# Performance work log

Measured on AMD Instinct MI355X. Metric: run time of the kernel, lower is better.

## Reference

```python
import jax, jax.numpy as jnp
import numpy as np

N = 50000      # nodes
E = 800000     # edges (avg degree 16)
IN = 128       # in_feats
OUT = 128      # out_feats
ASSIGN = 256   # assign_dim = B graphs * 8 clusters
B = 32         # batch_size (num graphs)


def setup_inputs() -> dict:
    key = jax.random.key(0)
    k0, k1, k2, k3 = jax.random.split(key, 4)
    x = jax.random.normal(k0, (N, IN), jnp.float32)
    edge_index = jax.random.randint(k1, (2, E), 0, N, dtype=jnp.int32)
    # sorted graph ids, ~equal-sized graphs (mirrors block_diag mask construction)
    batch = ((jnp.arange(N, dtype=jnp.int32) * B) // N).astype(jnp.int32)
    # SAGEConv params: Linear(2*in_feats -> out) on concat([x, mean_neigh])
    W_embed = jax.random.normal(k2, (2 * IN, OUT), jnp.float32) / np.float32(np.sqrt(2 * IN))
    b_embed = jnp.zeros((OUT,), jnp.float32)
    W_pool = jax.random.normal(k3, (2 * IN, ASSIGN), jnp.float32) / np.float32(np.sqrt(2 * IN))
    b_pool = jnp.zeros((ASSIGN,), jnp.float32)
    return dict(x=x, edge_index=edge_index, batch=batch,
                W_embed=W_embed, b_embed=b_embed, W_pool=W_pool, b_pool=b_pool)


def _sage(x, src, dst, W, b):
    # mean aggregation over in-neighbors (messages src -> dst), then Linear on concat
    n = x.shape[0]
    deg = jax.ops.segment_sum(jnp.ones((src.shape[0],), x.dtype), dst, num_segments=n)
    neigh = jax.ops.segment_sum(x[src], dst, num_segments=n) / jnp.maximum(deg, 1.0)[:, None]
    return jnp.concatenate([x, neigh], axis=-1) @ W + b


def reference(x, edge_index, batch, W_embed, b_embed, W_pool, b_pool):
    src, dst = edge_index[0], edge_index[1]
    embed = _sage(x, src, dst, W_embed, b_embed)                      # [N, OUT]
    pooled = jax.nn.softmax(_sage(x, src, dst, W_pool, b_pool), -1)   # [N, ASSIGN]
    # block-diagonal mask: node i of graph g sees columns [g*C, (g+1)*C)
    C = ASSIGN // B
    cols = jnp.arange(ASSIGN, dtype=batch.dtype) // C
    mask = (batch[:, None] == cols[None, :]).astype(x.dtype)          # [N, ASSIGN]
    # NOTE: faithful to original: softmax of (mask * pooled), zeros contribute exp(0)
    r = jax.nn.softmax(mask * pooled, axis=-1) * mask
    r = r / (r.sum(axis=-1, keepdims=True) + 1e-13)                   # [N, ASSIGN]
    h = r.T @ embed                                                   # [ASSIGN, OUT]
    # adj_new = S^T A S with A sparse COO (rows=edge_index[0], cols=edge_index[1])
    ar = jax.ops.segment_sum(r[dst], src, num_segments=x.shape[0])    # A @ S : [N, ASSIGN]
    adj_new = r.T @ ar                                                # [ASSIGN, ASSIGN]
    return (adj_new, h)
```

## Files before the change

### kernel.cpp

```cpp
#include <hip/hip_runtime.h>
#include <hip/hip_bf16.h>

#define N_ 50000
#define E_ 800000
#define IN_ 128
#define OUT_ 128
#define ASSIGN_ 256
#define B_ 32
#define KTOT 256
#define JTOT 384
#define HCHUNK 32
#define ACHUNK 32
#define AST 72
#define NXP ((N_ + 127) / 128)
#define NGB (NXP * 3)

#define NBKT 128
#define NPB 391
#define BCAP 7000
#define EPB 4096
#define NBLK_A ((E_ + EPB - 1) / EPB)

typedef __attribute__((ext_vector_type(8))) short short8;
typedef __attribute__((ext_vector_type(4))) float f32x4;
typedef __attribute__((ext_vector_type(2))) float f32x2;
typedef __attribute__((ext_vector_type(4))) unsigned short ushort4v;
typedef __attribute__((ext_vector_type(2))) unsigned short ushort2v;
typedef unsigned short u16;

__device__ inline unsigned short f2bf(float v) {
    union { float f; unsigned u; } a;
    a.f = v;
    unsigned r = a.u + 0x7fff + ((a.u >> 16) & 1);
    return (unsigned short)(r >> 16);
}
__device__ inline float bf2f(unsigned short b) {
    union { unsigned u; float f; } a;
    a.u = ((unsigned)b) << 16;
    return a.f;
}

__device__ inline unsigned enc8(float v) {
    union { float f; unsigned u; } a;
    a.f = v * 0x1p-120f;
    unsigned b = a.u;
    unsigned r = b + 0x7FFFF + ((b >> 20) & 1);
    return ((r >> 20) & 0x7F) | ((b >> 24) & 0x80);
}
__device__ inline float2 dec8x2(unsigned short p) {
#if defined(__has_builtin) && __has_builtin(__builtin_amdgcn_cvt_pk_f32_fp8)
    f32x2 r = __builtin_amdgcn_cvt_pk_f32_fp8((int)(unsigned)p, false);
    return make_float2(r.x, r.y);
#else
    unsigned u0 = p & 0xffu, u1 = (p >> 8) & 0xffu;
    union { unsigned u; float f; } a, b;
    a.u = ((u0 & 0x80u) << 24) | ((u0 & 0x7fu) << 20);
    b.u = ((u1 & 0x80u) << 24) | ((u1 & 0x7fu) << 20);
    return make_float2(a.f * 0x1p+120f, b.f * 0x1p+120f);
#endif
}

__global__ __launch_bounds__(256) void k_convx(const float* __restrict__ x,
                                               unsigned short* __restrict__ xhi,
                                               unsigned char* __restrict__ xq,
                                               int* __restrict__ bktFill) {
    if (blockIdx.x == 0 && threadIdx.x < NBKT) bktFill[threadIdx.x] = threadIdx.x * BCAP;
    int i4 = (blockIdx.x * 256 + threadIdx.x) * 4;
    if (i4 >= N_ * 128) return;
    float4 v = *(const float4*)(x + i4);
    ushort4v h;
    h.x = f2bf(v.x); h.y = f2bf(v.y); h.z = f2bf(v.z); h.w = f2bf(v.w);
    *(ushort4v*)(xhi + i4) = h;
    unsigned q = enc8(v.x) | (enc8(v.y) << 8) | (enc8(v.z) << 16) | (enc8(v.w) << 24);
    *(unsigned*)(xq + i4) = q;
}

__global__ __launch_bounds__(256) void k_binA(const int* __restrict__ ei,
                                              int* __restrict__ bktFill,
                                              int2* __restrict__ ebkt) {
    __shared__ int lh[NBKT], lbase[NBKT], lofs[NBKT];
    int t = threadIdx.x;
    int e0 = blockIdx.x * EPB;
    if (t < NBKT) { lh[t] = 0; lofs[t] = 0; }
    __syncthreads();
    int ss[16], dd[16];
#pragma unroll
    for (int i = 0; i < 16; i++) {
        int e = e0 + i * 256 + t;
        ss[i] = 0; dd[i] = -1;
        if (e < E_) {
            ss[i] = ei[e];
            dd[i] = ei[E_ + e];
            atomicAdd(&lh[dd[i] / NPB], 1);
        }
    }
    __syncthreads();
    if (t < NBKT) lbase[t] = atomicAdd(&bktFill[t], lh[t]);
    __syncthreads();
#pragma unroll
    for (int i = 0; i < 16; i++) {
        if (dd[i] >= 0) {
            int b = dd[i] / NPB;
            int o = atomicAdd(&lofs[b], 1);
            ebkt[lbase[b] + o] = make_int2(ss[i], dd[i]);
        }
    }
}

__global__ __launch_bounds__(256) void k_binB0(const int* __restrict__ bktFill,
                                               const int2* __restrict__ ebkt,
                                               int* __restrict__ locOff,
                                               int* __restrict__ bucketTotal) {
    __shared__ int ldeg[NPB];
    __shared__ int lscan[512];
    int b = blockIdx.x, t = threadIdx.x;
    for (int i = t; i < NPB; i += 256) ldeg[i] = 0;
    __syncthreads();
    int base = b * BCAP;
    int cnt = bktFill[b] - base;
    int n0 = b * NPB;
    for (int j = t; j < cnt; j += 256)
        atomicAdd(&ldeg[ebkt[base + j].y - n0], 1);
    __syncthreads();
    lscan[t] = (t < NPB) ? ldeg[t] : 0;
    lscan[t + 256] = (t + 256 < NPB) ? ldeg[t + 256] : 0;
    __syncthreads();
    for (int off = 1; off < 512; off <<= 1) {
        int x0 = lscan[t];
        int x1 = lscan[t + 256];
        int a0 = (t >= off) ? lscan[t - off] : 0;
        int a1 = (t + 256 >= off) ? lscan[t + 256 - off] : 0;
        __syncthreads();
        lscan[t] = x0 + a0;
        lscan[t + 256] = x1 + a1;
        __syncthreads();
    }
    for (int i = t; i < NPB; i += 256) {
        int n = n0 + i;
        if (n < N_) locOff[n] = (i == 0) ? 0 : lscan[i - 1];
    }
    if (t == 0) bucketTotal[b] = lscan[NPB - 1];
}

__global__ __launch_bounds__(128) void k_scanS(const int* __restrict__ bucketTotal,
                                               int* __restrict__ bucketBase,
                                               int* __restrict__ rowStart) {
    __shared__ int sh[128];
    int t = threadIdx.x;
    sh[t] = bucketTotal[t];
    __syncthreads();
    for (int off = 1; off < 128; off <<= 1) {
        int x = sh[t];
        int a = (t >= off) ? sh[t - off] : 0;
        __syncthreads();
        sh[t] = x + a;
        __syncthreads();
    }
    bucketBase[t] = (t == 0) ? 0 : sh[t - 1];
    if (t == 0) rowStart[N_] = E_;
}

__global__ __launch_bounds__(256) void k_binB1(const int* __restrict__ bktFill,
                                               const int2* __restrict__ ebkt,
                                               const int* __restrict__ locOff,
                                               const int* __restrict__ bucketBase,
                                               int* __restrict__ rowStart,
                                               int* __restrict__ csr_src,
                                               int* __restrict__ csr_dst) {
    __shared__ int lfill[NPB];
    int b = blockIdx.x, t = threadIdx.x;
    int base0 = bucketBase[b];
    int n0 = b * NPB;
    for (int i = t; i < NPB; i += 256) {
        int n = n0 + i;
        if (n < N_) {
            int lo = locOff[n];
            lfill[i] = lo;
            rowStart[n] = base0 + lo;
        }
    }
    __syncthreads();
    int base = b * BCAP;
    int cnt = bktFill[b] - base;
    for (int j = t; j < cnt; j += 256) {
        int2 sd = ebkt[base + j];
        int p = base0 + atomicAdd(&lfill[sd.y - n0], 1);
        csr_src[p] = sd.x;
        csr_dst[p] = sd.y;
    }
}

__global__ __launch_bounds__(256) void k_agg(const unsigned char* __restrict__ xq,
                                             const int* __restrict__ rowStart,
                                             const int* __restrict__ csr_src,
                                             unsigned short* __restrict__ nhi) {
    int node = blockIdx.x * 4 + (threadIdx.x >> 6);
    int lane = threadIdx.x & 63;
    if (node >= N_) return;
    int a = rowStart[node], bnd = rowStart[node + 1];
    float ax = 0.f, ay = 0.f;
    int j = a;
    for (; j + 3 < bnd; j += 4) {
        int s0 = csr_src[j], s1 = csr_src[j + 1];
        int s2 = csr_src[j + 2], s3 = csr_src[j + 3];
        unsigned short p0 = *(const unsigned short*)(xq + (size_t)s0 * 128 + lane * 2);
        unsigned short p1 = *(const unsigned short*)(xq + (size_t)s1 * 128 + lane * 2);
        unsigned short p2 = *(const unsigned short*)(xq + (size_t)s2 * 128 + lane * 2);
        unsigned short p3 = *(const unsigned short*)(xq + (size_t)s3 * 128 + lane * 2);
        float2 f0 = dec8x2(p0), f1 = dec8x2(p1), f2 = dec8x2(p2), f3 = dec8x2(p3);
        ax += (f0.x + f1.x) + (f2.x + f3.x);
        ay += (f0.y + f1.y) + (f2.y + f3.y);
    }
    for (; j < bnd; j++) {
        int s0 = csr_src[j];
        float2 f0 = dec8x2(*(const unsigned short*)(xq + (size_t)s0 * 128 + lane * 2));
        ax += f0.x;
        ay += f0.y;
    }
    float inv = 1.0f / (float)max(bnd - a, 1);
    ushort2v h;
    h.x = f2bf(ax * inv);
    h.y = f2bf(ay * inv);
    *(ushort2v*)(nhi + (size_t)node * 128 + lane * 2) = h;
}

__global__ void k_prep(const float* __restrict__ We, const float* __restrict__ be,
                       const float* __restrict__ Wp, const float* __restrict__ bp,
                       unsigned short* __restrict__ WThi, float* __restrict__ bias) {
    int idx = blockIdx.x * 256 + threadIdx.x;
    if (idx < JTOT * KTOT) {
        int j = idx / KTOT, k = idx - j * KTOT;
        float v = (j < 128) ? We[k * 128 + j] : Wp[k * 256 + (j - 128)];
        WThi[idx] = f2bf(v);
    }
    if (idx < JTOT) bias[idx] = (idx < 128) ? be[idx] : bp[idx - 128];
}

#define LDA 40
__global__ __launch_bounds__(256) void k_gemm(const unsigned short* __restrict__ xhi,
                                              const unsigned short* __restrict__ nhi,
                                              const unsigned short* __restrict__ WThi,
                                              const float* __restrict__ bias,
                                              unsigned short* __restrict__ embed,
                                              unsigned short* __restrict__ plog) {
    __shared__ __align__(16) union {
        struct { u16 Ah[128][LDA]; u16 Bh[128][LDA]; } s;
        u16 ep[64 * 128];
    } sm;
    int t = threadIdx.x;
    int wave = t >> 6, lane = t & 63;
    int wm = wave >> 1, wn = wave & 1;
    int q = lane >> 4, lr = lane & 15;

    int id = blockIdx.x;
    int xi, cc;
    if (id < (NXP / 8) * 24) {
        xi = (id / 24) * 8 + (id & 7);
        cc = (id % 24) >> 3;
    } else {
        int r2 = id - (NXP / 8) * 24;
        xi = (NXP / 8) * 8 + r2 % (NXP % 8);
        cc = r2 / (NXP % 8);
    }
    int row0 = xi * 128;
    int col0 = cc * 128;

    f32x4 acc[4][4] = {};
    int smr = t >> 1;
    int kc = (t & 1) * 16;

    for (int kt = 0; kt < KTOT; kt += 32) {
        const u16* Ah_src = (kt < 128) ? xhi : nhi;
        int kb = (kt & 127) + kc;
        int node = row0 + smr;
        short8 vh0 = {}, vh1 = {};
        if (node < N_) {
            const short8* ph = (const short8*)(Ah_src + (size_t)node * 128 + kb);
            vh0 = ph[0]; vh1 = ph[1];
        }
        *(short8*)&sm.s.Ah[smr][kc] = vh0;
        *(short8*)&sm.s.Ah[smr][kc + 8] = vh1;
        {
            const short8* ph = (const short8*)(WThi + (size_t)(col0 + smr) * 256 + kt + kc);
            short8 wh0 = ph[0], wh1 = ph[1];
            *(short8*)&sm.s.Bh[smr][kc] = wh0;
            *(short8*)&sm.s.Bh[smr][kc + 8] = wh1;
        }
        __syncthreads();

        short8 afh[4];
#pragma unroll
        for (int mi = 0; mi < 4; mi++) {
            int r = wm * 64 + mi * 16 + lr;
            afh[mi] = *(const short8*)&sm.s.Ah[r][q * 8];
        }
#pragma unroll
        for (int ni = 0; ni < 4; ni++) {
            int r = wn * 64 + ni * 16 + lr;
            short8 bfh = *(const short8*)&sm.s.Bh[r][q * 8];
#pragma unroll
            for (int mi = 0; mi < 4; mi++)
                acc[mi][ni] = __builtin_amdgcn_mfma_f32_16x16x32_bf16(afh[mi], bfh, acc[mi][ni], 0, 0, 0);
        }
        __syncthreads();
    }

    for (int half = 0; half < 2; half++) {
        __syncthreads();
        if (wm == half) {
#pragma unroll
            for (int mi = 0; mi < 4; mi++)
#pragma unroll
                for (int ni = 0; ni < 4; ni++) {
                    int lcol = wn * 64 + ni * 16 + lr;
                    float bj = bias[col0 + lcol];
#pragma unroll
                    for (int r = 0; r < 4; r++) {
                        int lrow = mi * 16 + q * 4 + r;
                        sm.ep[lrow * 128 + lcol] = f2bf(acc[mi][ni][r] + bj);
                    }
                }
        }
        __syncthreads();
#pragma unroll
        for (int i = 0; i < 4; i++) {
            int chunk = i * 256 + t;
            int lrow = chunk >> 4;
            int lco = (chunk & 15) * 8;
            int grow = row0 + half * 64 + lrow;
            if (grow < N_) {
                short8 v = *(const short8*)&sm.ep[lrow * 128 + lco];
                if (col0 < 128)
                    *(short8*)(embed + (size_t)grow * 128 + lco) = v;
                else
                    *(short8*)(plog + (size_t)grow * 256 + (col0 - 128) + lco) = v;
            }
        }
    }
}

__global__ __launch_bounds__(256) void k_r(const unsigned short* __restrict__ plog,
                                           const int* __restrict__ batch,
                                           float* __restrict__ r8,
                                           unsigned short* __restrict__ r8b) {
    int node = blockIdx.x * 4 + (threadIdx.x >> 6);
    int lane = threadIdx.x & 63;
    if (node >= N_) return;
    ushort4v p4 = *(const ushort4v*)(plog + (size_t)node * 256 + lane * 4);
    float px = bf2f(p4.x), py = bf2f(p4.y), pz = bf2f(p4.z), pw = bf2f(p4.w);
    float m = fmaxf(fmaxf(px, py), fmaxf(pz, pw));
    for (int off = 32; off; off >>= 1) m = fmaxf(m, __shfl_xor(m, off, 64));
    float s = expf(px - m) + expf(py - m) + expf(pz - m) + expf(pw - m);
    for (int off = 32; off; off >>= 1) s += __shfl_xor(s, off, 64);
    int g = batch[node];
    float v = 0.f;
    if (lane < 8) v = expf(bf2f(plog[(size_t)node * 256 + g * 8 + lane]) - m) / s;
    float M2 = v;
    for (int off = 4; off; off >>= 1) M2 = fmaxf(M2, __shfl_xor(M2, off, 64));
    float e = expf(v - M2);
    float Sg = e;
    for (int off = 4; off; off >>= 1) Sg += __shfl_xor(Sg, off, 64);
    float D2 = Sg + 248.0f * expf(-M2);
    float r = e / (Sg + 1e-13f * D2);
    if (lane < 8) {
        r8[node * 8 + lane] = r;
        r8b[node * 8 + lane] = f2bf(r);
    }
}

__global__ __launch_bounds__(256) void k_h_part(const unsigned short* __restrict__ embed,
                                                const float* __restrict__ r8,
                                                float* __restrict__ partH) {
    int g = blockIdx.x;
    int c = blockIdx.y;
    int t = threadIdx.x;
    int o = t & 127, half = t >> 7;
    int n0g = (g * N_ + 31) >> 5;
    int n1g = ((g + 1) * N_ + 31) >> 5;
    int len = n1g - n0g;
    int a = n0g + (len * c) / HCHUNK;
    int b = n0g + (len * (c + 1)) / HCHUNK;
    float a0 = 0.f, a1 = 0.f, a2 = 0.f, a3 = 0.f;
#pragma unroll 4
    for (int n = a; n < b; n++) {
        float e = bf2f(embed[(size_t)n * 128 + o]);
        const float* rr = r8 + n * 8 + half;
        a0 += rr[0] * e;
        a1 += rr[2] * e;
        a2 += rr[4] * e;
        a3 += rr[6] * e;
    }
    float* pb = partH + (g * HCHUNK + c) * 1024;
    pb[(half + 0) * 128 + o] = a0;
    pb[(half + 2) * 128 + o] = a1;
    pb[(half + 4) * 128 + o] = a2;
    pb[(half + 6) * 128 + o] = a3;
}

__global__ __launch_bounds__(256) void k_adjm(const int* __restrict__ rowStart,
                                              const int* __restrict__ csr_src,
                                              const int* __restrict__ csr_dst,
                                              const unsigned short* __restrict__ r8b,
                                              float* __restrict__ partAdj) {
    __shared__ __align__(16) unsigned short Ab[256 * AST];
    __shared__ __align__(16) unsigned short Bb[16 * AST];
    int gd = blockIdx.x, c = blockIdx.y;
    int t = threadIdx.x;
    int wave = t >> 6, lane = t & 63;
    int q = lane >> 4, lr = lane & 15;
    int n0g = (gd * N_ + 31) >> 5;
    int n1g = ((gd + 1) * N_ + 31) >> 5;
    int len = n1g - n0g;
    int na = n0g + (len * c) / ACHUNK;
    int nb = n0g + (len * (c + 1)) / ACHUNK;
    int j0 = rowStart[na], j1 = rowStart[nb];

    uint4 z = {0, 0, 0, 0};
#pragma unroll
    for (int i = 0; i < 9; i++) *(uint4*)&Ab[(i * 256 + t) * 8] = z;
    if (t < 144) *(uint4*)&Bb[t * 8] = z;
    __syncthreads();

    f32x4 acc[4] = {};
    int el = t >> 2;
    int ap = t & 3;

    for (int jt = j0; jt < j1; jt += 64) {
        int j = jt + el;
        int ca = -1;
        if (j < j1) {
            int s = csr_src[j];
            int d = csr_dst[j];
            int gs = (s * B_) / N_;
            unsigned sv = *(const unsigned*)(r8b + (size_t)s * 8 + ap * 2);
            unsigned dv = *(const unsigned*)(r8b + (size_t)d * 8 + ap * 2);
            ca = gs * 8 + ap * 2;
            Ab[ca * AST + el] = (unsigned short)sv;
            Ab[(ca + 1) * AST + el] = (unsigned short)(sv >> 16);
            Bb[(ap * 2) * AST + el] = (unsigned short)dv;
            Bb[(ap * 2 + 1) * AST + el] = (unsigned short)(dv >> 16);
        }
        __syncthreads();
        short8 bf0 = *(const short8*)&Bb[lr * AST + q * 8];
        short8 bf1 = *(const short8*)&Bb[lr * AST + 32 + q * 8];
#pragma unroll
        for (int mi = 0; mi < 4; mi++) {
            int col = (wave * 4 + mi) * 16 + lr;
            short8 a0 = *(const short8*)&Ab[col * AST + q * 8];
            short8 a1 = *(const short8*)&Ab[col * AST + 32 + q * 8];
            acc[mi] = __builtin_amdgcn_mfma_f32_16x16x32_bf16(a0, bf0, acc[mi], 0, 0, 0);
            acc[mi] = __builtin_amdgcn_mfma_f32_16x16x32_bf16(a1, bf1, acc[mi], 0, 0, 0);
        }
        __syncthreads();
        if (ca >= 0) {
            Ab[ca * AST + el] = 0;
            Ab[(ca + 1) * AST + el] = 0;
            Bb[(ap * 2) * AST + el] = 0;
            Bb[(ap * 2 + 1) * AST + el] = 0;
        }
        __syncthreads();
    }

    float* pb = partAdj + (gd * ACHUNK + c) * 2048;
    if (lr < 8) {
#pragma unroll
        for (int mi = 0; mi < 4; mi++) {
            int mbase = (wave * 4 + mi) * 16 + q * 4;
#pragma unroll
            for (int r = 0; r < 4; r++)
                pb[(mbase + r) * 8 + lr] = acc[mi][r];
        }
    }
}

__global__ __launch_bounds__(256) void k_red(const float* __restrict__ partAdj,
                                             const float* __restrict__ partH,
                                             float* __restrict__ out) {
    int o = blockIdx.x * 256 + threadIdx.x;
    if (o < 256 * 256) {
        int row = o >> 8, col = o & 255;
        int gd = col >> 3, b = col & 7;
        int li = row * 8 + b;
        float s = 0.f;
#pragma unroll
        for (int c = 0; c < ACHUNK; c++) s += partAdj[(gd * ACHUNK + c) * 2048 + li];
        out[o] = s;
    } else {
        int idx = o - 256 * 256;
        int g = idx >> 10;
        int local = idx & 1023;
        float s = 0.f;
#pragma unroll
        for (int c = 0; c < HCHUNK; c++) s += partH[(g * HCHUNK + c) * 1024 + local];
        out[256 * 256 + idx] = s;
    }
}

extern "C" void kernel_launch(void* const* d_in, const int* in_sizes, int n_in,
                              void* d_out, int out_size, void* d_ws, size_t ws_size,
                              hipStream_t stream) {
    const float* x = (const float*)d_in[0];
    const int* ei = (const int*)d_in[1];
    const int* batch = (const int*)d_in[2];
    const float* We = (const float*)d_in[3];
    const float* be = (const float*)d_in[4];
    const float* Wp = (const float*)d_in[5];
    const float* bp = (const float*)d_in[6];
    float* out = (float*)d_out;

    char* w = (char*)d_ws;
    auto alloc = [&](size_t bytes) -> char* {
        char* p = w;
        w += (bytes + 255) & ~(size_t)255;
        return p;
    };
    unsigned short* xhi = (unsigned short*)alloc((size_t)N_ * 128 * 2);
    unsigned char* xq = (unsigned char*)alloc((size_t)N_ * 128);
    unsigned short* nhi = (unsigned short*)alloc((size_t)N_ * 128 * 2);
    unsigned short* WThi = (unsigned short*)alloc((size_t)JTOT * KTOT * 2);
    unsigned short* embed = (unsigned short*)alloc((size_t)N_ * 128 * 2);
    unsigned short* plog = (unsigned short*)alloc((size_t)N_ * 256 * 2);
    float* r8 = (float*)alloc((size_t)N_ * 8 * 4);
    unsigned short* r8b = (unsigned short*)alloc((size_t)N_ * 8 * 2);
    float* bias = (float*)alloc(JTOT * 4);
    int* locOff = (int*)alloc((size_t)N_ * 4);
    int* rowStart = (int*)alloc((size_t)(N_ + 1) * 4);
    int* csr_src = (int*)alloc((size_t)E_ * 4);
    int* csr_dst = (int*)alloc((size_t)E_ * 4);
    int* bucketTotal = (int*)alloc(NBKT * 4);
    int* bucketBase = (int*)alloc(NBKT * 4);
    int* bktFill = (int*)alloc(NBKT * 4);
    int2* ebkt = (int2*)alloc((size_t)NBKT * BCAP * 8);
    float* partH = (float*)alloc((size_t)B_ * HCHUNK * 1024 * 4);
    float* partAdj = (float*)alloc((size_t)B_ * ACHUNK * 2048 * 4);

    k_convx<<<(N_ * 128 / 4 + 255) / 256, 256, 0, stream>>>(x, xhi, xq, bktFill);
    k_binA<<<NBLK_A, 256, 0, stream>>>(ei, bktFill, ebkt);
    k_binB0<<<NBKT, 256, 0, stream>>>(bktFill, ebkt, locOff, bucketTotal);
    k_scanS<<<1, 128, 0, stream>>>(bucketTotal, bucketBase, rowStart);
    k_binB1<<<NBKT, 256, 0, stream>>>(bktFill, ebkt, locOff, bucketBase, rowStart, csr_src, csr_dst);
    k_agg<<<(N_ + 3) / 4, 256, 0, stream>>>(xq, rowStart, csr_src, nhi);
    k_prep<<<(JTOT * KTOT + 255) / 256, 256, 0, stream>>>(We, be, Wp, bp, WThi, bias);
    k_gemm<<<NGB, 256, 0, stream>>>(xhi, nhi, WThi, bias, embed, plog);
    k_r<<<(N_ + 3) / 4, 256, 0, stream>>>(plog, batch, r8, r8b);
    k_h_part<<<dim3(B_, HCHUNK), 256, 0, stream>>>(embed, r8, partH);
    k_adjm<<<dim3(B_, ACHUNK), 256, 0, stream>>>(rowStart, csr_src, csr_dst, r8b, partAdj);
    k_red<<<(256 * 256 + 256 * 128 + 255) / 256, 256, 0, stream>>>(partAdj, partH, out);
}
```

Measured before the change: 247.5 us.

## Split fp8 feature table by halves per XCD and fold weight prep into convx

The fp8 copy of x is stored as two 64-feature half-tables. The aggregation kernel maps blocks so that the XCDs (taken as blockIdx mod 8) split into two groups, each gathering only one half, which shrinks the working set each XCD's L2 has to cache for random neighbor gathers. Each node is now handled by 32 lanes per half instead of 64 lanes over the full row. The weight transpose/bias prep kernel is merged into the conversion kernel as extra blocks, removing one launch. The risks are narrower 64-byte gathers per neighbor and reliance on round-robin block-to-XCD dispatch.

Result: no change. 244.8 us (-1.1%).

```diff
diff --git a/kernel.cpp b/kernel.cpp
--- a/kernel.cpp
+++ b/kernel.cpp
@@ -14,6 +14,8 @@
 #define AST 72
 #define NXP ((N_ + 127) / 128)
 #define NGB (NXP * 3)
+#define NCVX 6250
+#define NAGG (1563 * 8)
 
 #define NBKT 128
 #define NPB 391
@@ -63,16 +65,36 @@
 __global__ __launch_bounds__(256) void k_convx(const float* __restrict__ x,
                                                unsigned short* __restrict__ xhi,
                                                unsigned char* __restrict__ xq,
-                                               int* __restrict__ bktFill) {
-    if (blockIdx.x == 0 && threadIdx.x < NBKT) bktFill[threadIdx.x] = threadIdx.x * BCAP;
-    int i4 = (blockIdx.x * 256 + threadIdx.x) * 4;
+                                               int* __restrict__ bktFill,
+                                               const float* __restrict__ We,
+                                               const float* __restrict__ be,
+                                               const float* __restrict__ Wp,
+                                               const float* __restrict__ bp,
+                                               unsigned short* __restrict__ WThi,
+                                               float* __restrict__ bias) {
+    int bid = blockIdx.x;
+    int t = threadIdx.x;
+    if (bid >= NCVX) {
+        int idx = (bid - NCVX) * 256 + t;
+        if (idx < JTOT * KTOT) {
+            int j = idx / KTOT, k = idx - j * KTOT;
+            float v = (j < 128) ? We[k * 128 + j] : Wp[k * 256 + (j - 128)];
+            WThi[idx] = f2bf(v);
+        }
+        if (idx < JTOT) bias[idx] = (idx < 128) ? be[idx] : bp[idx - 128];
+        return;
+    }
+    if (bid == 0 && t < NBKT) bktFill[t] = t * BCAP;
+    int i4 = (bid * 256 + t) * 4;
     if (i4 >= N_ * 128) return;
     float4 v = *(const float4*)(x + i4);
     ushort4v h;
     h.x = f2bf(v.x); h.y = f2bf(v.y); h.z = f2bf(v.z); h.w = f2bf(v.w);
     *(ushort4v*)(xhi + i4) = h;
     unsigned q = enc8(v.x) | (enc8(v.y) << 8) | (enc8(v.z) << 16) | (enc8(v.w) << 24);
-    *(unsigned*)(xq + i4) = q;
+    int f = i4 & 127, node = i4 >> 7;
+    int half = f >> 6, fo = f & 63;
+    *(unsigned*)(xq + ((size_t)half * N_ + node) * 64 + fo) = q;
 }
 
 __global__ __launch_bounds__(256) void k_binA(const int* __restrict__ ei,
@@ -194,26 +216,32 @@
                                              const int* __restrict__ rowStart,
                                              const int* __restrict__ csr_src,
                                              unsigned short* __restrict__ nhi) {
-    int node = blockIdx.x * 4 + (threadIdx.x >> 6);
-    int lane = threadIdx.x & 63;
+    int b = blockIdx.x;
+    int xcd = b & 7;
+    int half = xcd >> 2;
+    int gi = (b >> 3) * 4 + (xcd & 3);
+    int t = threadIdx.x;
+    int node = gi * 8 + (t >> 5);
+    int l = t & 31;
     if (node >= N_) return;
+    const unsigned char* base = xq + (size_t)half * N_ * 64;
     int a = rowStart[node], bnd = rowStart[node + 1];
     float ax = 0.f, ay = 0.f;
     int j = a;
     for (; j + 3 < bnd; j += 4) {
         int s0 = csr_src[j], s1 = csr_src[j + 1];
         int s2 = csr_src[j + 2], s3 = csr_src[j + 3];
-        unsigned short p0 = *(const unsigned short*)(xq + (size_t)s0 * 128 + lane * 2);
-        unsigned short p1 = *(const unsigned short*)(xq + (size_t)s1 * 128 + lane * 2);
-        unsigned short p2 = *(const unsigned short*)(xq + (size_t)s2 * 128 + lane * 2);
-        unsigned short p3 = *(const unsigned short*)(xq + (size_t)s3 * 128 + lane * 2);
+        unsigned short p0 = *(const unsigned short*)(base + (size_t)s0 * 64 + l * 2);
+        unsigned short p1 = *(const unsigned short*)(base + (size_t)s1 * 64 + l * 2);
+        unsigned short p2 = *(const unsigned short*)(base + (size_t)s2 * 64 + l * 2);
+        unsigned short p3 = *(const unsigned short*)(base + (size_t)s3 * 64 + l * 2);
         float2 f0 = dec8x2(p0), f1 = dec8x2(p1), f2 = dec8x2(p2), f3 = dec8x2(p3);
         ax += (f0.x + f1.x) + (f2.x + f3.x);
         ay += (f0.y + f1.y) + (f2.y + f3.y);
     }
     for (; j < bnd; j++) {
         int s0 = csr_src[j];
-        float2 f0 = dec8x2(*(const unsigned short*)(xq + (size_t)s0 * 128 + lane * 2));
+        float2 f0 = dec8x2(*(const unsigned short*)(base + (size_t)s0 * 64 + l * 2));
         ax += f0.x;
         ay += f0.y;
     }
@@ -221,19 +249,7 @@
     ushort2v h;
     h.x = f2bf(ax * inv);
     h.y = f2bf(ay * inv);
-    *(ushort2v*)(nhi + (size_t)node * 128 + lane * 2) = h;
-}
-
-__global__ void k_prep(const float* __restrict__ We, const float* __restrict__ be,
-                       const float* __restrict__ Wp, const float* __restrict__ bp,
-                       unsigned short* __restrict__ WThi, float* __restrict__ bias) {
-    int idx = blockIdx.x * 256 + threadIdx.x;
-    if (idx < JTOT * KTOT) {
-        int j = idx / KTOT, k = idx - j * KTOT;
-        float v = (j < 128) ? We[k * 128 + j] : Wp[k * 256 + (j - 128)];
-        WThi[idx] = f2bf(v);
-    }
-    if (idx < JTOT) bias[idx] = (idx < 128) ? be[idx] : bp[idx - 128];
+    *(ushort2v*)(nhi + (size_t)node * 128 + half * 64 + l * 2) = h;
 }
 
 #define LDA 40
@@ -534,13 +550,12 @@
     float* partH = (float*)alloc((size_t)B_ * HCHUNK * 1024 * 4);
     float* partAdj = (float*)alloc((size_t)B_ * ACHUNK * 2048 * 4);
 
-    k_convx<<<(N_ * 128 / 4 + 255) / 256, 256, 0, stream>>>(x, xhi, xq, bktFill);
+    k_convx<<<NCVX + 384, 256, 0, stream>>>(x, xhi, xq, bktFill, We, be, Wp, bp, WThi, bias);
     k_binA<<<NBLK_A, 256, 0, stream>>>(ei, bktFill, ebkt);
     k_binB0<<<NBKT, 256, 0, stream>>>(bktFill, ebkt, locOff, bucketTotal);
     k_scanS<<<1, 128, 0, stream>>>(bucketTotal, bucketBase, rowStart);
     k_binB1<<<NBKT, 256, 0, stream>>>(bktFill, ebkt, locOff, bucketBase, rowStart, csr_src, csr_dst);
-    k_agg<<<(N_ + 3) / 4, 256, 0, stream>>>(xq, rowStart, csr_src, nhi);
-    k_prep<<<(JTOT * KTOT + 255) / 256, 256, 0, stream>>>(We, be, Wp, bp, WThi, bias);
+    k_agg<<<NAGG, 256, 0, stream>>>(xq, rowStart, csr_src, nhi);
     k_gemm<<<NGB, 256, 0, stream>>>(xhi, nhi, WThi, bias, embed, plog);
     k_r<<<(N_ + 3) / 4, 256, 0, stream>>>(plog, batch, r8, r8b);
     k_h_part<<<dim3(B_, HCHUNK), 256, 0, stream>>>(embed, r8, partH);
```

## Merge preprocessing and tail kernels, fold bucket scan, widen neighbor-aggregation loads

Applied to the files above, without the earlier changes.

Merges the x conversion, edge binning and weight prep into one heterogeneous launch, and merges the h-partial and adjacency-partial kernels into one launch. The tiny bucket-offset scan moves inside k_binB1, with a memset replacing the in-kernel bktFill init. The aggregation kernel now has each half-wave handle a different edge with 4-byte loads, giving more edges in flight per iteration. The aim is fewer launches and less launch/tail overhead, at the cost of a redundant per-block scan and mixed-work blocks that may balance unevenly.

Measured after the change: 228.5 us. 1.08x faster.

```diff
diff --git a/kernel.cpp b/kernel.cpp
--- a/kernel.cpp
+++ b/kernel.cpp
@@ -14,12 +14,14 @@
 #define AST 72
 #define NXP ((N_ + 127) / 128)
 #define NGB (NXP * 3)
+#define NCVX 6250
 
 #define NBKT 128
 #define NPB 391
 #define BCAP 7000
 #define EPB 4096
 #define NBLK_A ((E_ + EPB - 1) / EPB)
+#define NPRE (NBLK_A + NCVX + 384)
 
 typedef __attribute__((ext_vector_type(8))) short short8;
 typedef __attribute__((ext_vector_type(4))) float f32x4;
@@ -60,12 +62,60 @@
 #endif
 }
 
-__global__ __launch_bounds__(256) void k_convx(const float* __restrict__ x,
-                                               unsigned short* __restrict__ xhi,
-                                               unsigned char* __restrict__ xq,
-                                               int* __restrict__ bktFill) {
-    if (blockIdx.x == 0 && threadIdx.x < NBKT) bktFill[threadIdx.x] = threadIdx.x * BCAP;
-    int i4 = (blockIdx.x * 256 + threadIdx.x) * 4;
+__global__ __launch_bounds__(256) void k_pre(const int* __restrict__ ei,
+                                             int* __restrict__ bktFill,
+                                             int2* __restrict__ ebkt,
+                                             const float* __restrict__ x,
+                                             unsigned short* __restrict__ xhi,
+                                             unsigned char* __restrict__ xq,
+                                             const float* __restrict__ We,
+                                             const float* __restrict__ be,
+                                             const float* __restrict__ Wp,
+                                             const float* __restrict__ bp,
+                                             unsigned short* __restrict__ WThi,
+                                             float* __restrict__ bias) {
+    __shared__ int lh[NBKT], lbase[NBKT], lofs[NBKT];
+    int bid = blockIdx.x;
+    int t = threadIdx.x;
+    if (bid < NBLK_A) {
+        int e0 = bid * EPB;
+        if (t < NBKT) { lh[t] = 0; lofs[t] = 0; }
+        __syncthreads();
+        int ss[16], dd[16];
+#pragma unroll
+        for (int i = 0; i < 16; i++) {
+            int e = e0 + i * 256 + t;
+            ss[i] = 0; dd[i] = -1;
+            if (e < E_) {
+                ss[i] = ei[e];
+                dd[i] = ei[E_ + e];
+                atomicAdd(&lh[dd[i] / NPB], 1);
+            }
+        }
+        __syncthreads();
+        if (t < NBKT) lbase[t] = t * BCAP + atomicAdd(&bktFill[t], lh[t]);
+        __syncthreads();
+#pragma unroll
+        for (int i = 0; i < 16; i++) {
+            if (dd[i] >= 0) {
+                int b = dd[i] / NPB;
+                int o = atomicAdd(&lofs[b], 1);
+                ebkt[lbase[b] + o] = make_int2(ss[i], dd[i]);
+            }
+        }
+        return;
+    }
+    if (bid >= NBLK_A + NCVX) {
+        int idx = (bid - NBLK_A - NCVX) * 256 + t;
+        if (idx < JTOT * KTOT) {
+            int j = idx / KTOT, k = idx - j * KTOT;
+            float v = (j < 128) ? We[k * 128 + j] : Wp[k * 256 + (j - 128)];
+            WThi[idx] = f2bf(v);
+        }
+        if (idx < JTOT) bias[idx] = (idx < 128) ? be[idx] : bp[idx - 128];
+        return;
+    }
+    int i4 = ((bid - NBLK_A) * 256 + t) * 4;
     if (i4 >= N_ * 128) return;
     float4 v = *(const float4*)(x + i4);
     ushort4v h;
@@ -73,38 +123,6 @@
     *(ushort4v*)(xhi + i4) = h;
     unsigned q = enc8(v.x) | (enc8(v.y) << 8) | (enc8(v.z) << 16) | (enc8(v.w) << 24);
     *(unsigned*)(xq + i4) = q;
-}
-
-__global__ __launch_bounds__(256) void k_binA(const int* __restrict__ ei,
-                                              int* __restrict__ bktFill,
-                                              int2* __restrict__ ebkt) {
-    __shared__ int lh[NBKT], lbase[NBKT], lofs[NBKT];
-    int t = threadIdx.x;
-    int e0 = blockIdx.x * EPB;
-    if (t < NBKT) { lh[t] = 0; lofs[t] = 0; }
-    __syncthreads();
-    int ss[16], dd[16];
-#pragma unroll
-    for (int i = 0; i < 16; i++) {
-        int e = e0 + i * 256 + t;
-        ss[i] = 0; dd[i] = -1;
-        if (e < E_) {
-            ss[i] = ei[e];
-            dd[i] = ei[E_ + e];
-            atomicAdd(&lh[dd[i] / NPB], 1);
-        }
-    }
-    __syncthreads();
-    if (t < NBKT) lbase[t] = atomicAdd(&bktFill[t], lh[t]);
-    __syncthreads();
-#pragma unroll
-    for (int i = 0; i < 16; i++) {
-        if (dd[i] >= 0) {
-            int b = dd[i] / NPB;
-            int o = atomicAdd(&lofs[b], 1);
-            ebkt[lbase[b] + o] = make_int2(ss[i], dd[i]);
-        }
-    }
 }
 
 __global__ __launch_bounds__(256) void k_binB0(const int* __restrict__ bktFill,
@@ -117,7 +135,7 @@
     for (int i = t; i < NPB; i += 256) ldeg[i] = 0;
     __syncthreads();
     int base = b * BCAP;
-    int cnt = bktFill[b] - base;
+    int cnt = bktFill[b];
     int n0 = b * NPB;
     for (int j = t; j < cnt; j += 256)
         atomicAdd(&ldeg[ebkt[base + j].y - n0], 1);
@@ -142,34 +160,26 @@
     if (t == 0) bucketTotal[b] = lscan[NPB - 1];
 }
 
-__global__ __launch_bounds__(128) void k_scanS(const int* __restrict__ bucketTotal,
-                                               int* __restrict__ bucketBase,
-                                               int* __restrict__ rowStart) {
-    __shared__ int sh[128];
-    int t = threadIdx.x;
-    sh[t] = bucketTotal[t];
-    __syncthreads();
-    for (int off = 1; off < 128; off <<= 1) {
-        int x = sh[t];
-        int a = (t >= off) ? sh[t - off] : 0;
-        __syncthreads();
-        sh[t] = x + a;
-        __syncthreads();
-    }
-    bucketBase[t] = (t == 0) ? 0 : sh[t - 1];
-    if (t == 0) rowStart[N_] = E_;
-}
-
 __global__ __launch_bounds__(256) void k_binB1(const int* __restrict__ bktFill,
                                                const int2* __restrict__ ebkt,
                                                const int* __restrict__ locOff,
-                                               const int* __restrict__ bucketBase,
+                                               const int* __restrict__ bucketTotal,
                                                int* __restrict__ rowStart,
                                                int* __restrict__ csr_src,
                                                int* __restrict__ csr_dst) {
     __shared__ int lfill[NPB];
+    __shared__ int bsc[NBKT];
     int b = blockIdx.x, t = threadIdx.x;
-    int base0 = bucketBase[b];
+    if (t < NBKT) bsc[t] = bucketTotal[t];
+    __syncthreads();
+    for (int off = 1; off < NBKT; off <<= 1) {
+        int x = (t < NBKT) ? bsc[t] : 0;
+        int add = (t < NBKT && t >= off) ? bsc[t - off] : 0;
+        __syncthreads();
+        if (t < NBKT) bsc[t] = x + add;
+        __syncthreads();
+    }
+    int base0 = (b == 0) ? 0 : bsc[b - 1];
     int n0 = b * NPB;
     for (int i = t; i < NPB; i += 256) {
         int n = n0 + i;
@@ -181,13 +191,14 @@
     }
     __syncthreads();
     int base = b * BCAP;
-    int cnt = bktFill[b] - base;
+    int cnt = bktFill[b];
     for (int j = t; j < cnt; j += 256) {
         int2 sd = ebkt[base + j];
         int p = base0 + atomicAdd(&lfill[sd.y - n0], 1);
         csr_src[p] = sd.x;
         csr_dst[p] = sd.y;
     }
+    if (b == 0 && t == 0) rowStart[N_] = E_;
 }
 
 __global__ __launch_bounds__(256) void k_agg(const unsigned char* __restrict__ xq,
@@ -195,45 +206,51 @@
                                              const int* __restrict__ csr_src,
                                              unsigned short* __restrict__ nhi) {
     int node = blockIdx.x * 4 + (threadIdx.x >> 6);
+    if (node >= N_) return;
     int lane = threadIdx.x & 63;
-    if (node >= N_) return;
+    int l5 = lane & 31;
+    int eh = lane >> 5;
     int a = rowStart[node], bnd = rowStart[node + 1];
-    float ax = 0.f, ay = 0.f;
+    float a0 = 0.f, a1 = 0.f, a2 = 0.f, a3 = 0.f;
     int j = a;
-    for (; j + 3 < bnd; j += 4) {
-        int s0 = csr_src[j], s1 = csr_src[j + 1];
-        int s2 = csr_src[j + 2], s3 = csr_src[j + 3];
-        unsigned short p0 = *(const unsigned short*)(xq + (size_t)s0 * 128 + lane * 2);
-        unsigned short p1 = *(const unsigned short*)(xq + (size_t)s1 * 128 + lane * 2);
-        unsigned short p2 = *(const unsigned short*)(xq + (size_t)s2 * 128 + lane * 2);
-        unsigned short p3 = *(const unsigned short*)(xq + (size_t)s3 * 128 + lane * 2);
-        float2 f0 = dec8x2(p0), f1 = dec8x2(p1), f2 = dec8x2(p2), f3 = dec8x2(p3);
-        ax += (f0.x + f1.x) + (f2.x + f3.x);
-        ay += (f0.y + f1.y) + (f2.y + f3.y);
-    }
-    for (; j < bnd; j++) {
-        int s0 = csr_src[j];
-        float2 f0 = dec8x2(*(const unsigned short*)(xq + (size_t)s0 * 128 + lane * 2));
-        ax += f0.x;
-        ay += f0.y;
-    }
+    for (; j + 7 < bnd; j += 8) {
+        unsigned q[4];
+#pragma unroll
+        for (int ii = 0; ii < 4; ii++) {
+            int s = csr_src[j + 2 * ii + eh];
+            q[ii] = *(const unsigned*)(xq + (size_t)s * 128 + l5 * 4);
+        }
+#pragma unroll
+        for (int ii = 0; ii < 4; ii++) {
+            float2 f01 = dec8x2((unsigned short)(q[ii] & 0xffffu));
+            float2 f23 = dec8x2((unsigned short)(q[ii] >> 16));
+            a0 += f01.x; a1 += f01.y; a2 += f23.x; a3 += f23.y;
+        }
+    }
+    for (; j < bnd; j += 2) {
+        unsigned qq = 0;
+        int e = j + eh;
+        if (e < bnd) {
+            int s = csr_src[e];
+            qq = *(const unsigned*)(xq + (size_t)s * 128 + l5 * 4);
+        }
+        float2 f01 = dec8x2((unsigned short)(qq & 0xffffu));
+        float2 f23 = dec8x2((unsigned short)(qq >> 16));
+        a0 += f01.x; a1 += f01.y; a2 += f23.x; a3 += f23.y;
+    }
+    a0 += __shfl_xor(a0, 32, 64);
+    a1 += __shfl_xor(a1, 32, 64);
+    a2 += __shfl_xor(a2, 32, 64);
+    a3 += __shfl_xor(a3, 32, 64);
     float inv = 1.0f / (float)max(bnd - a, 1);
-    ushort2v h;
-    h.x = f2bf(ax * inv);
-    h.y = f2bf(ay * inv);
-    *(ushort2v*)(nhi + (size_t)node * 128 + lane * 2) = h;
-}
-
-__global__ void k_prep(const float* __restrict__ We, const float* __restrict__ be,
-                       const float* __restrict__ Wp, const float* __restrict__ bp,
-                       unsigned short* __restrict__ WThi, float* __restrict__ bias) {
-    int idx = blockIdx.x * 256 + threadIdx.x;
-    if (idx < JTOT * KTOT) {
-        int j = idx / KTOT, k = idx - j * KTOT;
-        float v = (j < 128) ? We[k * 128 + j] : Wp[k * 256 + (j - 128)];
-        WThi[idx] = f2bf(v);
-    }
-    if (idx < JTOT) bias[idx] = (idx < 128) ? be[idx] : bp[idx - 128];
+    if (lane < 32) {
+        ushort4v h;
+        h.x = f2bf(a0 * inv);
+        h.y = f2bf(a1 * inv);
+        h.z = f2bf(a2 * inv);
+        h.w = f2bf(a3 * inv);
+        *(ushort4v*)(nhi + (size_t)node * 128 + l5 * 4) = h;
+    }
 }
 
 #define LDA 40
@@ -368,44 +385,47 @@
     }
 }
 
-__global__ __launch_bounds__(256) void k_h_part(const unsigned short* __restrict__ embed,
-                                                const float* __restrict__ r8,
-                                                float* __restrict__ partH) {
-    int g = blockIdx.x;
-    int c = blockIdx.y;
-    int t = threadIdx.x;
-    int o = t & 127, half = t >> 7;
-    int n0g = (g * N_ + 31) >> 5;
-    int n1g = ((g + 1) * N_ + 31) >> 5;
-    int len = n1g - n0g;
-    int a = n0g + (len * c) / HCHUNK;
-    int b = n0g + (len * (c + 1)) / HCHUNK;
-    float a0 = 0.f, a1 = 0.f, a2 = 0.f, a3 = 0.f;
-#pragma unroll 4
-    for (int n = a; n < b; n++) {
-        float e = bf2f(embed[(size_t)n * 128 + o]);
-        const float* rr = r8 + n * 8 + half;
-        a0 += rr[0] * e;
-        a1 += rr[2] * e;
-        a2 += rr[4] * e;
-        a3 += rr[6] * e;
-    }
-    float* pb = partH + (g * HCHUNK + c) * 1024;
-    pb[(half + 0) * 128 + o] = a0;
-    pb[(half + 2) * 128 + o] = a1;
-    pb[(half + 4) * 128 + o] = a2;
-    pb[(half + 6) * 128 + o] = a3;
-}
-
-__global__ __launch_bounds__(256) void k_adjm(const int* __restrict__ rowStart,
+__global__ __launch_bounds__(256) void k_tail(const int* __restrict__ rowStart,
                                               const int* __restrict__ csr_src,
                                               const int* __restrict__ csr_dst,
                                               const unsigned short* __restrict__ r8b,
-                                              float* __restrict__ partAdj) {
+                                              float* __restrict__ partAdj,
+                                              const unsigned short* __restrict__ embed,
+                                              const float* __restrict__ r8,
+                                              float* __restrict__ partH) {
     __shared__ __align__(16) unsigned short Ab[256 * AST];
     __shared__ __align__(16) unsigned short Bb[16 * AST];
-    int gd = blockIdx.x, c = blockIdx.y;
+    int id = blockIdx.x;
     int t = threadIdx.x;
+    if (id >= B_ * ACHUNK) {
+        int idh = id - B_ * ACHUNK;
+        int g = idh & 31;
+        int c = idh >> 5;
+        int o = t & 127, half = t >> 7;
+        int n0g = (g * N_ + 31) >> 5;
+        int n1g = ((g + 1) * N_ + 31) >> 5;
+        int len = n1g - n0g;
+        int a = n0g + (len * c) / HCHUNK;
+        int b = n0g + (len * (c + 1)) / HCHUNK;
+        float a0 = 0.f, a1 = 0.f, a2 = 0.f, a3 = 0.f;
+#pragma unroll 4
+        for (int n = a; n < b; n++) {
+            float e = bf2f(embed[(size_t)n * 128 + o]);
+            const float* rr = r8 + n * 8 + half;
+            a0 += rr[0] * e;
+            a1 += rr[2] * e;
+            a2 += rr[4] * e;
+            a3 += rr[6] * e;
+        }
+        float* pb = partH + (g * HCHUNK + c) * 1024;
+        pb[(half + 0) * 128 + o] = a0;
+        pb[(half + 2) * 128 + o] = a1;
+        pb[(half + 4) * 128 + o] = a2;
+        pb[(half + 6) * 128 + o] = a3;
+        return;
+    }
+    int gd = id & 31;
+    int c = id >> 5;
     int wave = t >> 6, lane = t & 63;
     int q = lane >> 4, lr = lane & 15;
     int n0g = (gd * N_ + 31) >> 5;
@@ -528,22 +548,18 @@
     int* csr_src = (int*)alloc((size_t)E_ * 4);
     int* csr_dst = (int*)alloc((size_t)E_ * 4);
     int* bucketTotal = (int*)alloc(NBKT * 4);
-    int* bucketBase = (int*)alloc(NBKT * 4);
     int* bktFill = (int*)alloc(NBKT * 4);
     int2* ebkt = (int2*)alloc((size_t)NBKT * BCAP * 8);
     float* partH = (float*)alloc((size_t)B_ * HCHUNK * 1024 * 4);
     float* partAdj = (float*)alloc((size_t)B_ * ACHUNK * 2048 * 4);
 
-    k_convx<<<(N_ * 128 / 4 + 255) / 256, 256, 0, stream>>>(x, xhi, xq, bktFill);
-    k_binA<<<NBLK_A, 256, 0, stream>>>(ei, bktFill, ebkt);
+    hipMemsetAsync(bktFill, 0, NBKT * 4, stream);
+    k_pre<<<NPRE, 256, 0, stream>>>(ei, bktFill, ebkt, x, xhi, xq, We, be, Wp, bp, WThi, bias);
     k_binB0<<<NBKT, 256, 0, stream>>>(bktFill, ebkt, locOff, bucketTotal);
-    k_scanS<<<1, 128, 0, stream>>>(bucketTotal, bucketBase, rowStart);
-    k_binB1<<<NBKT, 256, 0, stream>>>(bktFill, ebkt, locOff, bucketBase, rowStart, csr_src, csr_dst);
+    k_binB1<<<NBKT, 256, 0, stream>>>(bktFill, ebkt, locOff, bucketTotal, rowStart, csr_src, csr_dst);
     k_agg<<<(N_ + 3) / 4, 256, 0, stream>>>(xq, rowStart, csr_src, nhi);
-    k_prep<<<(JTOT * KTOT + 255) / 256, 256, 0, stream>>>(We, be, Wp, bp, WThi, bias);
     k_gemm<<<NGB, 256, 0, stream>>>(xhi, nhi, WThi, bias, embed, plog);
     k_r<<<(N_ + 3) / 4, 256, 0, stream>>>(plog, batch, r8, r8b);
-    k_h_part<<<dim3(B_, HCHUNK), 256, 0, stream>>>(embed, r8, partH);
-    k_adjm<<<dim3(B_, ACHUNK), 256, 0, stream>>>(rowStart, csr_src, csr_dst, r8b, partAdj);
+    k_tail<<<2 * B_ * ACHUNK, 256, 0, stream>>>(rowStart, csr_src, csr_dst, r8b, partAdj, embed, r8, partH);
     k_red<<<(256 * 256 + 256 * 128 + 255) / 256, 256, 0, stream>>>(partAdj, partH, out);
 }
```
